# Performance work log

Hardware: AMD Instinct MI355X
Metric: run time of the kernel (lower is better)

Reference implementation:

```python
import jax, jax.numpy as jnp
import numpy as np
from jax import lax

H = 50  # hidden size fixed by the module


def setup_inputs() -> dict:
    key = jax.random.key(0)
    ks = jax.random.split(key, 7)
    B, T, I = 512, 1000, 64
    s = 0.1
    return {
        "x": jax.random.normal(ks[0], (B, T, I), dtype=jnp.float32),
        "W_ih": jax.random.normal(ks[1], (4 * H, I), dtype=jnp.float32) * s,
        "W_hh": jax.random.normal(ks[2], (4 * H, H), dtype=jnp.float32) * s,
        "b_ih": jax.random.normal(ks[3], (4 * H,), dtype=jnp.float32) * s,
        "b_hh": jax.random.normal(ks[4], (4 * H,), dtype=jnp.float32) * s,
        "W_out": jax.random.normal(ks[5], (2, H), dtype=jnp.float32) * s,
        "b_out": jax.random.normal(ks[6], (2,), dtype=jnp.float32) * s,
    }


def _lstm_last_h(x, W_ih, W_hh, b_ih, b_hh):
    # x: [B, T, I]. Precompute input contribution to all gates: [B, T, 4H]
    xg = jnp.einsum("bti,gi->btg", x, W_ih) + b_ih + b_hh
    B = x.shape[0]
    h0 = jnp.zeros((B, H), dtype=x.dtype)
    c0 = jnp.zeros((B, H), dtype=x.dtype)

    def step(carry, xt):
        h, c = carry
        gates = xt + h @ W_hh.T  # [B, 4H]
        i, f, g, o = jnp.split(gates, 4, axis=-1)  # torch gate order i,f,g,o
        i = jax.nn.sigmoid(i)
        f = jax.nn.sigmoid(f)
        g = jnp.tanh(g)
        o = jax.nn.sigmoid(o)
        c = f * c + i * g
        h = o * jnp.tanh(c)
        return (h, c), None

    (h_last, _), _ = lax.scan(step, (h0, c0), jnp.swapaxes(xg, 0, 1))
    return h_last  # [B, H]


def reference(x, W_ih, W_hh, b_ih, b_hh, W_out, b_out):
    h = _lstm_last_h(x, W_ih, W_hh, b_ih, b_hh)
    return h @ W_out.T + b_out  # [B, 2]
```

## Files before the change

kernel.cpp:

```cpp
#include <hip/hip_runtime.h>
#include <math.h>


#define HSZ 50
#define ISZ 64
#define TSZ 1000

typedef float f32x2 __attribute__((ext_vector_type(2)));

__device__ __forceinline__ float dpp_xor1(float v) {
    return __int_as_float(__builtin_amdgcn_update_dpp(
        0, __float_as_int(v), 0xB1, 0xF, 0xF, true));
}
__device__ __forceinline__ float dpp_xor2(float v) {
    return __int_as_float(__builtin_amdgcn_update_dpp(
        0, __float_as_int(v), 0x4E, 0xF, 0xF, true));
}
__device__ __forceinline__ float dpp_rev(float v) {
    return __int_as_float(__builtin_amdgcn_update_dpp(
        0, __float_as_int(v), 0x1B, 0xF, 0xF, true));
}

#define LSTM_STEP(t, OFF, XR, XG)                                              \
  {                                                                            \
    if (tid < 200) {                                                           \
                                      \
      f32x2 accA; accA.x = XG; accA.y = 0.0f;                                  \
      f32x2 accB; accB.x = 0.0f; accB.y = 0.0f;                                \
      const float4* h4 = (const float4*)(&hbuf[(OFF) & 1][0]);                 \
      _Pragma("unroll")                                                        \
      for (int j = 0; j < 12; ++j) {                                           \
        float4 v = h4[j];                                                      \
        f32x2 lo; lo.x = v.x; lo.y = v.y;                                      \
        f32x2 hi; hi.x = v.z; hi.y = v.w;                                      \
        accA += lo * whh[2 * j];                                               \
        accB += hi * whh[2 * j + 1];                                           \
      }                                                                        \
      { f32x2 tl = *(const f32x2*)(&hbuf[(OFF) & 1][48]);                      \
        accA += tl * whh[24]; }                                                \
      float acc = (accA.x + accB.x) + (accA.y + accB.y);                       \
      float e  = __expf(-(acc * gmul));                                        \
      float sg = __builtin_amdgcn_rcpf(1.0f + e);                              \
      float a  = __builtin_fmaf(sg, gma, gmb);            \
      float fg = dpp_xor1(a);                                                  \
      float gg = dpp_xor2(a);                                                  \
      float og = dpp_rev(a);                                                   \
      c_reg = __builtin_fmaf(fg, c_reg, a * gg);      \
      float ep = __expf(2.0f * c_reg);                                         \
      float rr = __builtin_amdgcn_rcpf(1.0f + ep);                             \
      float hv = __builtin_fmaf(-2.0f * og, rr, og);         \
      if ((tid & 3) == 0) hbuf[((OFF) + 1) & 1][u] = hv;                       \
            \
      if ((t) + (OFF) + 2 < TSZ) {                                             \
        f32x2 pA; pA.x = bias; pA.y = 0.0f;                                    \
        f32x2 pB; pB.x = 0.0f; pB.y = 0.0f;                                    \
        const float4* x4 = (const float4*)(&xbuf[((OFF) + 2) & 3][0]);         \
        _Pragma("unroll")                                                      \
        for (int i = 0; i < 16; ++i) {                                         \
          float4 v = x4[i];                                                    \
          f32x2 lo; lo.x = v.x; lo.y = v.y;                                    \
          f32x2 hi; hi.x = v.z; hi.y = v.w;                                    \
          pA += lo * wih[2 * i];                                               \
          pB += hi * wih[2 * i + 1];                                           \
        }                                                                      \
        XG = (pA.x + pB.x) + (pA.y + pB.y);                                    \
      }                                                                        \
    } else if (tid >= 224) {                                                   \
      if ((t) + (OFF) + 3 < TSZ)                                               \
        *(f32x2*)(&xbuf[((OFF) + 3) & 3][2 * ll]) = XR;                        \
      if ((t) + (OFF) + 7 < TSZ)                                               \
        XR = *(const f32x2*)(xrow + (size_t)((t) + (OFF) + 7) * ISZ + 2 * ll); \
    }                                                                          \
                     \
    asm volatile("s_waitcnt lgkmcnt(0)" ::: "memory");                         \
    __builtin_amdgcn_s_barrier();                                              \
    __builtin_amdgcn_sched_barrier(0);                                         \
  }

__global__ __launch_bounds__(256, 2) void lstm_fused(
    const float* __restrict__ x,
    const float* __restrict__ W_ih,
    const float* __restrict__ W_hh,
    const float* __restrict__ b_ih,
    const float* __restrict__ b_hh,
    const float* __restrict__ W_out,
    const float* __restrict__ b_out,
    float* __restrict__ out)
{
    const int row = blockIdx.x;
    const int tid = threadIdx.x;

    __shared__ __align__(16) float xbuf[4][ISZ];
    __shared__ __align__(16) float hbuf[2][56];

    const int g = tid & 3;
    const int u = tid >> 2;
    const int k = g * HSZ + u;
    const float gmul = (g == 2) ? 2.0f : 1.0f;
    const float gma  = (g == 2) ? 2.0f : 1.0f;
    const float gmb  = (g == 2) ? -1.0f : 0.0f;

    const int ll = tid - 224;

    const float* xrow = x + (size_t)row * (TSZ * ISZ);

    f32x2 whh[25];
    f32x2 wih[32];
    float bias  = 0.0f;
    float c_reg = 0.0f;
    float xgE = 0.0f, xgO = 0.0f;
    f32x2 xr0{}, xr1{}, xr2{}, xr3{};

    if (tid < 200) {
        const float* wh = W_hh + k * HSZ;
        #pragma unroll
        for (int j = 0; j < 25; ++j) whh[j] = *(const f32x2*)(wh + 2 * j);
        const float* wi = W_ih + k * ISZ;
        #pragma unroll
        for (int i = 0; i < 32; ++i) wih[i] = *(const f32x2*)(wi + 2 * i);
        bias = b_ih[k] + b_hh[k];
    } else if (ll >= 0) {
        #pragma unroll
        for (int n = 0; n < 3; ++n) {
            *(f32x2*)(&xbuf[n][2 * ll]) =
                *(const f32x2*)(xrow + (size_t)n * ISZ + 2 * ll);
        }
        xr0 = *(const f32x2*)(xrow + 3 * (size_t)ISZ + 2 * ll);
        xr1 = *(const f32x2*)(xrow + 4 * (size_t)ISZ + 2 * ll);
        xr2 = *(const f32x2*)(xrow + 5 * (size_t)ISZ + 2 * ll);
        xr3 = *(const f32x2*)(xrow + 6 * (size_t)ISZ + 2 * ll);
    }
    if (tid < 56) { hbuf[0][tid] = 0.0f; hbuf[1][tid] = 0.0f; }
    __syncthreads();

    if (tid < 200) {
        #pragma unroll
        for (int n = 0; n < 2; ++n) {
            f32x2 pA; pA.x = bias; pA.y = 0.0f;
            f32x2 pB; pB.x = 0.0f; pB.y = 0.0f;
            const float4* x4 = (const float4*)(&xbuf[n][0]);
            #pragma unroll
            for (int i = 0; i < 16; ++i) {
                float4 v = x4[i];
                f32x2 lo; lo.x = v.x; lo.y = v.y;
                f32x2 hi; hi.x = v.z; hi.y = v.w;
                pA += lo * wih[2 * i];
                pB += hi * wih[2 * i + 1];
            }
            float r = (pA.x + pB.x) + (pA.y + pB.y);
            if (n == 0) xgE = r; else xgO = r;
        }
    }

    for (int t = 0; t < TSZ; t += 4) {
        LSTM_STEP(t, 0, xr0, xgE)
        LSTM_STEP(t, 1, xr1, xgO)
        LSTM_STEP(t, 2, xr2, xgE)
        LSTM_STEP(t, 3, xr3, xgO)
    }

    if (tid < 2) {
        float acc = b_out[tid];
        const float* wo = W_out + tid * HSZ;
        #pragma unroll
        for (int j = 0; j < HSZ; ++j) acc += hbuf[0][j] * wo[j];
        out[row * 2 + tid] = acc;
    }
}

extern "C" void kernel_launch(void* const* d_in, const int* in_sizes, int n_in,
                              void* d_out, int out_size, void* d_ws, size_t ws_size,
                              hipStream_t stream) {
    const float* x     = (const float*)d_in[0];
    const float* W_ih  = (const float*)d_in[1];
    const float* W_hh  = (const float*)d_in[2];
    const float* b_ih  = (const float*)d_in[3];
    const float* b_hh  = (const float*)d_in[4];
    const float* W_out = (const float*)d_in[5];
    const float* b_out = (const float*)d_in[6];
    float* out = (float*)d_out;

    const int B = in_sizes[0] / (TSZ * ISZ);
    hipLaunchKernelGGL(lstm_fused, dim3(B), dim3(256), 0, stream,
                       x, W_ih, W_hh, b_ih, b_hh, W_out, b_out, out);
}
```

Measured before the change: 759.4 us.

## Restructure LSTM block into specialized waves with one lane per hidden unit

Gives each of the four waves a role. One wave computes all four gates of a hidden unit per lane (50 lanes), holding all W_hh rows in registers and removing the DPP cross-lane gate exchange. Two waves compute the input projections into a shared xg ring buffer, and one wave streams x from global memory. Wave roles rotate by block index so the recurrent wave lands on different SIMDs across co-resident blocks. The cost is four times the serial recurrent work per lane on the critical path and higher register pressure (200 floats of weights), against fewer active lanes and less cross-lane traffic.

```diff
diff --git a/kernel.cpp b/kernel.cpp
--- a/kernel.cpp
+++ b/kernel.cpp
@@ -8,70 +8,75 @@
 
 typedef float f32x2 __attribute__((ext_vector_type(2)));
 
-__device__ __forceinline__ float dpp_xor1(float v) {
-    return __int_as_float(__builtin_amdgcn_update_dpp(
-        0, __float_as_int(v), 0xB1, 0xF, 0xF, true));
-}
-__device__ __forceinline__ float dpp_xor2(float v) {
-    return __int_as_float(__builtin_amdgcn_update_dpp(
-        0, __float_as_int(v), 0x4E, 0xF, 0xF, true));
-}
-__device__ __forceinline__ float dpp_rev(float v) {
-    return __int_as_float(__builtin_amdgcn_update_dpp(
-        0, __float_as_int(v), 0x1B, 0xF, 0xF, true));
-}
-
-#define LSTM_STEP(t, OFF, XR, XG)                                              \
+#define LSTM_STEP(t, OFF, XR)                                                  \
   {                                                                            \
-    if (tid < 200) {                                                           \
-                                      \
-      f32x2 accA; accA.x = XG; accA.y = 0.0f;                                  \
-      f32x2 accB; accB.x = 0.0f; accB.y = 0.0f;                                \
-      const float4* h4 = (const float4*)(&hbuf[(OFF) & 1][0]);                 \
-      _Pragma("unroll")                                                        \
-      for (int j = 0; j < 12; ++j) {                                           \
-        float4 v = h4[j];                                                      \
-        f32x2 lo; lo.x = v.x; lo.y = v.y;                                      \
-        f32x2 hi; hi.x = v.z; hi.y = v.w;                                      \
-        accA += lo * whh[2 * j];                                               \
-        accB += hi * whh[2 * j + 1];                                           \
+    if (lw == 0) {                                                             \
+      if (lane < HSZ) {                                                        \
+                   \
+        float xgi = xgring[(OFF) & 3][lane];                                   \
+        float xgf = xgring[(OFF) & 3][HSZ + lane];                             \
+        float xgg = xgring[(OFF) & 3][2 * HSZ + lane];                         \
+        float xgo = xgring[(OFF) & 3][3 * HSZ + lane];                         \
+        f32x2 acc0; acc0.x = xgi; acc0.y = 0.0f;                               \
+        f32x2 acc1; acc1.x = xgf; acc1.y = 0.0f;                               \
+        f32x2 acc2; acc2.x = xgg; acc2.y = 0.0f;                               \
+        f32x2 acc3; acc3.x = xgo; acc3.y = 0.0f;                               \
+        const float4* h4 = (const float4*)(&hbuf[(OFF) & 1][0]);               \
+        _Pragma("unroll")                                                      \
+        for (int j = 0; j < 12; ++j) {                                         \
+          float4 v = h4[j];                                                    \
+          f32x2 lo; lo.x = v.x; lo.y = v.y;                                    \
+          f32x2 hi; hi.x = v.z; hi.y = v.w;                                    \
+          acc0 += lo * wreg[2 * j];          acc0 += hi * wreg[2 * j + 1];     \
+          acc1 += lo * wreg[25 + 2 * j];     acc1 += hi * wreg[25 + 2 * j + 1];\
+          acc2 += lo * wreg[50 + 2 * j];     acc2 += hi * wreg[50 + 2 * j + 1];\
+          acc3 += lo * wreg[75 + 2 * j];     acc3 += hi * wreg[75 + 2 * j + 1];\
+        }                                                                      \
+        { f32x2 tl = *(const f32x2*)(&hbuf[(OFF) & 1][48]);                    \
+          acc0 += tl * wreg[24]; acc1 += tl * wreg[49];                        \
+          acc2 += tl * wreg[74]; acc3 += tl * wreg[99]; }                      \
+        float s0 = acc0.x + acc0.y, s1 = acc1.x + acc1.y;                      \
+        float s2 = acc2.x + acc2.y, s3 = acc3.x + acc3.y;                      \
+              \
+        float e0 = __expf(-s0), e1 = __expf(-s1);                              \
+        float e2 = __expf(-2.0f * s2), e3 = __expf(-s3);                       \
+        float i_ = __builtin_amdgcn_rcpf(1.0f + e0);                           \
+        float f_ = __builtin_amdgcn_rcpf(1.0f + e1);                           \
+        float g_ = __builtin_fmaf(2.0f, __builtin_amdgcn_rcpf(1.0f + e2),      \
+                                  -1.0f);                                      \
+        float o_ = __builtin_amdgcn_rcpf(1.0f + e3);                           \
+        c_reg = __builtin_fmaf(f_, c_reg, i_ * g_);                            \
+        float ec = __expf(2.0f * c_reg);                                       \
+        float rr = __builtin_amdgcn_rcpf(1.0f + ec);                           \
+        float hv = o_ * __builtin_fmaf(-2.0f, rr, 1.0f);        \
+        hbuf[((OFF) + 1) & 1][lane] = hv;                                      \
       }                                                                        \
-      { f32x2 tl = *(const f32x2*)(&hbuf[(OFF) & 1][48]);                      \
-        accA += tl * whh[24]; }                                                \
-      float acc = (accA.x + accB.x) + (accA.y + accB.y);                       \
-      float e  = __expf(-(acc * gmul));                                        \
-      float sg = __builtin_amdgcn_rcpf(1.0f + e);                              \
-      float a  = __builtin_fmaf(sg, gma, gmb);            \
-      float fg = dpp_xor1(a);                                                  \
-      float gg = dpp_xor2(a);                                                  \
-      float og = dpp_rev(a);                                                   \
-      c_reg = __builtin_fmaf(fg, c_reg, a * gg);      \
-      float ep = __expf(2.0f * c_reg);                                         \
-      float rr = __builtin_amdgcn_rcpf(1.0f + ep);                             \
-      float hv = __builtin_fmaf(-2.0f * og, rr, og);         \
-      if ((tid & 3) == 0) hbuf[((OFF) + 1) & 1][u] = hv;                       \
-            \
+    } else if (lw <= 2) {                                                      \
       if ((t) + (OFF) + 2 < TSZ) {                                             \
-        f32x2 pA; pA.x = bias; pA.y = 0.0f;                                    \
-        f32x2 pB; pB.x = 0.0f; pB.y = 0.0f;                                    \
-        const float4* x4 = (const float4*)(&xbuf[((OFF) + 2) & 3][0]);         \
+        const float4* x4 = (const float4*)(&xring[((OFF) + 2) & 3][0]);        \
+        f32x2 a1; a1.x = bias0; a1.y = 0.0f;                                   \
+        f32x2 b1; b1.x = 0.0f; b1.y = 0.0f;                                    \
+        f32x2 a2; a2.x = bias1; a2.y = 0.0f;                                   \
+        f32x2 b2; b2.x = 0.0f; b2.y = 0.0f;                                    \
         _Pragma("unroll")                                                      \
         for (int i = 0; i < 16; ++i) {                                         \
           float4 v = x4[i];                                                    \
           f32x2 lo; lo.x = v.x; lo.y = v.y;                                    \
           f32x2 hi; hi.x = v.z; hi.y = v.w;                                    \
-          pA += lo * wih[2 * i];                                               \
-          pB += hi * wih[2 * i + 1];                                           \
+          a1 += lo * wreg[2 * i];      b1 += hi * wreg[2 * i + 1];             \
+          a2 += lo * wreg[32 + 2 * i]; b2 += hi * wreg[32 + 2 * i + 1];        \
         }                                                                      \
-        XG = (pA.x + pB.x) + (pA.y + pB.y);                                    \
+        xgring[((OFF) + 2) & 3][k1] = (a1.x + b1.x) + (a1.y + b1.y);           \
+        if (pid < 72)                                                          \
+          xgring[((OFF) + 2) & 3][k1 + 128] = (a2.x + b2.x) + (a2.y + b2.y);   \
       }                                                                        \
-    } else if (tid >= 224) {                                                   \
+    } else if (lane < 32) {                                                    \
       if ((t) + (OFF) + 3 < TSZ)                                               \
-        *(f32x2*)(&xbuf[((OFF) + 3) & 3][2 * ll]) = XR;                        \
+        *(f32x2*)(&xring[((OFF) + 3) & 3][2 * lane]) = XR;                     \
       if ((t) + (OFF) + 7 < TSZ)                                               \
-        XR = *(const f32x2*)(xrow + (size_t)((t) + (OFF) + 7) * ISZ + 2 * ll); \
+        XR = *(const f32x2*)(xrow + (size_t)((t) + (OFF) + 7) * ISZ + 2*lane); \
     }                                                                          \
-                     \
+              \
     asm volatile("s_waitcnt lgkmcnt(0)" ::: "memory");                         \
     __builtin_amdgcn_s_barrier();                                              \
     __builtin_amdgcn_sched_barrier(0);                                         \
@@ -87,76 +92,98 @@
     const float* __restrict__ b_out,
     float* __restrict__ out)
 {
-    const int row = blockIdx.x;
-    const int tid = threadIdx.x;
-
-    __shared__ __align__(16) float xbuf[4][ISZ];
-    __shared__ __align__(16) float hbuf[2][56];
-
-    const int g = tid & 3;
-    const int u = tid >> 2;
-    const int k = g * HSZ + u;
-    const float gmul = (g == 2) ? 2.0f : 1.0f;
-    const float gma  = (g == 2) ? 2.0f : 1.0f;
-    const float gmb  = (g == 2) ? -1.0f : 0.0f;
-
-    const int ll = tid - 224;
+    const int row  = blockIdx.x;
+    const int tid  = threadIdx.x;
+    const int lane = tid & 63;
+    const int pw   = tid >> 6;
+    const int rot  = (row + (row >> 8)) & 3;
+    const int lw   = (pw + rot) & 3;
+
+    __shared__ __align__(16) float xring[4][ISZ];
+    __shared__ __align__(16) float xgring[4][200];
+    __shared__ __align__(16) float hbuf[2][52];
 
     const float* xrow = x + (size_t)row * (TSZ * ISZ);
 
-    f32x2 whh[25];
-    f32x2 wih[32];
-    float bias  = 0.0f;
+    f32x2 wreg[100];
+    float bias0 = 0.0f, bias1 = 0.0f;
     float c_reg = 0.0f;
-    float xgE = 0.0f, xgO = 0.0f;
-    f32x2 xr0{}, xr1{}, xr2{}, xr3{};
-
-    if (tid < 200) {
-        const float* wh = W_hh + k * HSZ;
-        #pragma unroll
-        for (int j = 0; j < 25; ++j) whh[j] = *(const f32x2*)(wh + 2 * j);
-        const float* wi = W_ih + k * ISZ;
-        #pragma unroll
-        for (int i = 0; i < 32; ++i) wih[i] = *(const f32x2*)(wi + 2 * i);
-        bias = b_ih[k] + b_hh[k];
-    } else if (ll >= 0) {
-        #pragma unroll
-        for (int n = 0; n < 3; ++n) {
-            *(f32x2*)(&xbuf[n][2 * ll]) =
-                *(const f32x2*)(xrow + (size_t)n * ISZ + 2 * ll);
+    f32x2 xr0; xr0.x = 0.0f; xr0.y = 0.0f;
+    f32x2 xr1; xr1.x = 0.0f; xr1.y = 0.0f;
+    f32x2 xr2; xr2.x = 0.0f; xr2.y = 0.0f;
+    f32x2 xr3; xr3.x = 0.0f; xr3.y = 0.0f;
+    int pid = 0, k1 = 0;
+
+    if (lw == 0) {
+        if (lane < HSZ) {
+            #pragma unroll
+            for (int g = 0; g < 4; ++g) {
+                const float* wh = W_hh + (g * HSZ + lane) * HSZ;
+                #pragma unroll
+                for (int p = 0; p < 25; ++p)
+                    wreg[g * 25 + p] = *(const f32x2*)(wh + 2 * p);
+            }
         }
-        xr0 = *(const f32x2*)(xrow + 3 * (size_t)ISZ + 2 * ll);
-        xr1 = *(const f32x2*)(xrow + 4 * (size_t)ISZ + 2 * ll);
-        xr2 = *(const f32x2*)(xrow + 5 * (size_t)ISZ + 2 * ll);
-        xr3 = *(const f32x2*)(xrow + 6 * (size_t)ISZ + 2 * ll);
-    }
-    if (tid < 56) { hbuf[0][tid] = 0.0f; hbuf[1][tid] = 0.0f; }
+    } else if (lw <= 2) {
+        pid = (lw - 1) * 64 + lane;
+        k1  = pid;
+        const float* wi = W_ih + (size_t)k1 * ISZ;
+        #pragma unroll
+        for (int i = 0; i < 32; ++i) wreg[i] = *(const f32x2*)(wi + 2 * i);
+        bias0 = b_ih[k1] + b_hh[k1];
+        if (pid < 72) {
+            const float* wi2 = W_ih + (size_t)(k1 + 128) * ISZ;
+            #pragma unroll
+            for (int i = 0; i < 32; ++i)
+                wreg[32 + i] = *(const f32x2*)(wi2 + 2 * i);
+            bias1 = b_ih[k1 + 128] + b_hh[k1 + 128];
+        } else {
+            #pragma unroll
+            for (int i = 0; i < 32; ++i) {
+                wreg[32 + i].x = 0.0f; wreg[32 + i].y = 0.0f;
+            }
+        }
+    } else if (lane < 32) {
+        #pragma unroll
+        for (int n = 0; n < 3; ++n)
+            *(f32x2*)(&xring[n][2 * lane]) =
+                *(const f32x2*)(xrow + (size_t)n * ISZ + 2 * lane);
+        xr0 = *(const f32x2*)(xrow + 3 * (size_t)ISZ + 2 * lane);
+        xr1 = *(const f32x2*)(xrow + 4 * (size_t)ISZ + 2 * lane);
+        xr2 = *(const f32x2*)(xrow + 5 * (size_t)ISZ + 2 * lane);
+        xr3 = *(const f32x2*)(xrow + 6 * (size_t)ISZ + 2 * lane);
+    }
+    if (tid < 52) { hbuf[0][tid] = 0.0f; hbuf[1][tid] = 0.0f; }
     __syncthreads();
 
-    if (tid < 200) {
+    if (lw == 1 || lw == 2) {
         #pragma unroll
         for (int n = 0; n < 2; ++n) {
-            f32x2 pA; pA.x = bias; pA.y = 0.0f;
-            f32x2 pB; pB.x = 0.0f; pB.y = 0.0f;
-            const float4* x4 = (const float4*)(&xbuf[n][0]);
+            const float4* x4 = (const float4*)(&xring[n][0]);
+            f32x2 a1; a1.x = bias0; a1.y = 0.0f;
+            f32x2 b1; b1.x = 0.0f; b1.y = 0.0f;
+            f32x2 a2; a2.x = bias1; a2.y = 0.0f;
+            f32x2 b2; b2.x = 0.0f; b2.y = 0.0f;
             #pragma unroll
             for (int i = 0; i < 16; ++i) {
                 float4 v = x4[i];
                 f32x2 lo; lo.x = v.x; lo.y = v.y;
                 f32x2 hi; hi.x = v.z; hi.y = v.w;
-                pA += lo * wih[2 * i];
-                pB += hi * wih[2 * i + 1];
+                a1 += lo * wreg[2 * i];      b1 += hi * wreg[2 * i + 1];
+                a2 += lo * wreg[32 + 2 * i]; b2 += hi * wreg[32 + 2 * i + 1];
             }
-            float r = (pA.x + pB.x) + (pA.y + pB.y);
-            if (n == 0) xgE = r; else xgO = r;
+            xgring[n][k1] = (a1.x + b1.x) + (a1.y + b1.y);
+            if (pid < 72)
+                xgring[n][k1 + 128] = (a2.x + b2.x) + (a2.y + b2.y);
         }
     }
+    __syncthreads();
 
     for (int t = 0; t < TSZ; t += 4) {
-        LSTM_STEP(t, 0, xr0, xgE)
-        LSTM_STEP(t, 1, xr1, xgO)
-        LSTM_STEP(t, 2, xr2, xgE)
-        LSTM_STEP(t, 3, xr3, xgO)
+        LSTM_STEP(t, 0, xr0)
+        LSTM_STEP(t, 1, xr1)
+        LSTM_STEP(t, 2, xr2)
+        LSTM_STEP(t, 3, xr3)
     }
 
     if (tid < 2) {
```

Result: slower. 1.624 ms (+113.8%).
